# Performance work log

Measured on AMD Instinct MI355X. Metric: run time of the kernel, lower is better.

## Reference

```python
import jax, jax.numpy as jnp
import numpy as np

WINDOW_SIZE = 11
SIGMA = 1.5
CHANNEL = 3


def _gaussian_window(window_size, sigma, channel):
    x = np.arange(window_size, dtype=np.float32)
    g = np.exp(-((x - window_size // 2) ** 2) / (2.0 * sigma ** 2))
    g = g / g.sum()
    w2d = np.outer(g, g).astype(np.float32)  # (ws, ws)
    # depthwise kernel: (C, 1, ws, ws) in OIHW with feature_group_count=C
    return jnp.asarray(np.broadcast_to(w2d, (channel, 1, window_size, window_size)).copy())


def _dwconv(x, w, pad):
    # x: (N, C, H, W), w: (C, 1, kh, kw), depthwise 'same' conv
    return jax.lax.conv_general_dilated(
        x, w, window_strides=(1, 1), padding=[(pad, pad), (pad, pad)],
        dimension_numbers=("NCHW", "OIHW", "NCHW"),
        feature_group_count=x.shape[1])


def setup_inputs() -> dict:
    key = jax.random.key(0)
    k1, k2 = jax.random.split(key)
    img1 = jax.random.uniform(k1, (32, 3, 512, 512), dtype=jnp.float32)
    img2 = jax.random.uniform(k2, (32, 3, 512, 512), dtype=jnp.float32)
    window = _gaussian_window(WINDOW_SIZE, SIGMA, CHANNEL)
    return {"img1": img1, "img2": img2, "window": window}


def reference(img1, img2, window):
    pad = WINDOW_SIZE // 2
    mu1 = _dwconv(img1, window, pad)
    mu2 = _dwconv(img2, window, pad)
    mu1_sq = mu1 * mu1
    mu2_sq = mu2 * mu2
    mu1_mu2 = mu1 * mu2
    sigma1_sq = _dwconv(img1 * img1, window, pad) - mu1_sq
    sigma2_sq = _dwconv(img2 * img2, window, pad) - mu2_sq
    sigma12 = _dwconv(img1 * img2, window, pad) - mu1_mu2

    C1 = 0.01 ** 2
    C2 = 0.03 ** 2
    C3 = C2 / 2.0

    a1 = jnp.abs(sigma1_sq)
    a2 = jnp.abs(sigma2_sq)
    s1 = jnp.sqrt(a1)
    s2 = jnp.sqrt(a2)

    L = (2.0 * mu1_mu2 + C1) / (mu1_sq + mu2_sq + C1)
    C = (2.0 * s1 * s2 + C2) / (a1 + a2 + C2)
    S = (sigma12 + C3) / (s1 * s2 + C3)

    return (L.mean(), C.mean(), S.mean())
```

## Files before the change

### kernel.cpp

```cpp
#include <hip/hip_runtime.h>
#include <math.h>

#define IMG 512
#define PLANES 96
#define XS_W 54
#define NXS 10
#define YS_H 128
#define NYS 4
#define WPB 4
#define NBLK ((PLANES * NXS * NYS) / WPB)
#define INV_NPIX (1.0 / 25165824.0)


static __device__ __forceinline__ float rflf(float x) {
    return __int_as_float(__builtin_amdgcn_readfirstlane(__float_as_int(x)));
}

static __device__ __forceinline__ float dpp_shr1(float x) {
    return __int_as_float(__builtin_amdgcn_mov_dpp(__float_as_int(x), 0x138, 0xF, 0xF, true));
}
static __device__ __forceinline__ float dpp_shl1(float x) {
    return __int_as_float(__builtin_amdgcn_mov_dpp(__float_as_int(x), 0x130, 0xF, 0xF, true));
}

template<int P, int BSEL, bool EMIT>
__device__ __forceinline__ void row_step(
    int T, int y0, bool col_ok,
    const float* __restrict__ p1, const float* __restrict__ p2,
    float& xe1, float& xe2, float& xo1, float& xo2,
    const float (&g)[11],
    float (&A)[5][11], bool out_ok, float& sL, float& sC, float& sS)
{
    const int t = T + P;
    float& x1r = BSEL ? xo1 : xe1;
    float& x2r = BSEL ? xo2 : xe2;
    const int gy2 = y0 - 3 + t;
    float nx1 = 0.f, nx2 = 0.f;
    if (col_ok && (unsigned)gy2 < IMG) {
        int off = gy2 * IMG;
        nx1 = p1[off];
        nx2 = p2[off];
    }
    const float x1 = x1r, x2 = x2r;
    float a4 = dpp_shr1(x1), b4 = dpp_shr1(x2);
    float a3 = dpp_shr1(a4), b3 = dpp_shr1(b4);
    float a2 = dpp_shr1(a3), b2r = dpp_shr1(b3);
    float a1 = dpp_shr1(a2), b1r = dpp_shr1(b2r);
    float a0 = dpp_shr1(a1), b0 = dpp_shr1(b1r);
    float t1 = g[0] * a0, t2 = g[0] * b0;
    float H1 = t1, H2 = t2;
    float H11 = t1 * a0, H22 = t2 * b0, H12 = t1 * b0;
#define HACC(J, AJ, BJ)                                   \
    t1 = g[J] * (AJ); t2 = g[J] * (BJ);                   \
    H1 += t1; H2 += t2;                                   \
    H11 = fmaf(t1, (AJ), H11);                            \
    H22 = fmaf(t2, (BJ), H22);                            \
    H12 = fmaf(t1, (BJ), H12);
    HACC(1, a1, b1r)
    HACC(2, a2, b2r)
    HACC(3, a3, b3)
    HACC(4, a4, b4)
    HACC(5, x1, x2)
    float ar = dpp_shl1(x1), br = dpp_shl1(x2);
    HACC(6, ar, br)
    ar = dpp_shl1(ar); br = dpp_shl1(br);
    HACC(7, ar, br)
    ar = dpp_shl1(ar); br = dpp_shl1(br);
    HACC(8, ar, br)
    ar = dpp_shl1(ar); br = dpp_shl1(br);
    HACC(9, ar, br)
    ar = dpp_shl1(ar); br = dpp_shl1(br);
    HACC(10, ar, br)
#undef HACC
    #pragma unroll
    for (int j = 0; j < 11; ++j) {
        const int s = (P + j + 1) % 11;
        float w = g[10 - j];
        if (j == 10) {
            A[0][s] = w * H1;
            A[1][s] = w * H2;
            A[2][s] = w * H11;
            A[3][s] = w * H22;
            A[4][s] = w * H12;
        } else {
            A[0][s] = fmaf(w, H1,  A[0][s]);
            A[1][s] = fmaf(w, H2,  A[1][s]);
            A[2][s] = fmaf(w, H11, A[2][s]);
            A[3][s] = fmaf(w, H22, A[3][s]);
            A[4][s] = fmaf(w, H12, A[4][s]);
        }
    }
    if (EMIT) {
        const int es = (P + 1) % 11;
        float mu1 = A[0][es], mu2 = A[1][es];
        float x11 = A[2][es], x22 = A[3][es], x12 = A[4][es];
        float mu1s = mu1 * mu1, mu2s = mu2 * mu2, mu12 = mu1 * mu2;
        float v1 = x11 - mu1s, v2 = x22 - mu2s, v12 = x12 - mu12;
        float q1 = fabsf(v1), q2 = fabsf(v2);
        float q12 = sqrtf(q1 * q2);
        const float C1 = 1e-4f, C2 = 9e-4f, C3 = 4.5e-4f;
        float eL = __fdividef(2.f * mu12 + C1, mu1s + mu2s + C1);
        float eC = __fdividef(2.f * q12 + C2, q1 + q2 + C2);
        float eS = __fdividef(v12 + C3, q12 + C3);
        if (out_ok) { sL += eL; sC += eC; sS += eS; }
    }
    x1r = nx1; x2r = nx2;
}

#define RS(Tc, Pc, Bc, Ec) \
    row_step<Pc, Bc, Ec>(Tc, y0, col_ok, p1, p2, xe1, xe2, xo1, xo2, g, A, out_ok, sL, sC, sS)

__global__ __launch_bounds__(256, 4) void ssim_main(
    const float* __restrict__ img1, const float* __restrict__ img2,
    const float* __restrict__ win, float4* __restrict__ part)
{
    const int lane = threadIdx.x & 63;
    const int widx = threadIdx.x >> 6;
    const int wid  = blockIdx.x * WPB + widx;
    const int plane = wid / (NXS * NYS);
    const int rem   = wid % (NXS * NYS);
    const int ys = rem / NXS, xs = rem % NXS;
    const int x0 = xs * XS_W;
    const int y0 = ys * YS_H;
    const int col = x0 - 5 + lane;
    const bool col_ok = (unsigned)col < IMG;
    const bool out_ok = (lane >= 5) && (lane <= 58) && col_ok;

    float g[11];
    #pragma unroll
    for (int j = 0; j < 11; ++j) g[j] = rflf(sqrtf(win[j * 12]));

    const float* p1 = img1 + (size_t)plane * (IMG * IMG) + col;
    const float* p2 = img2 + (size_t)plane * (IMG * IMG) + col;

    float xe1 = 0.f, xe2 = 0.f, xo1 = 0.f, xo2 = 0.f;
    {
        int gy = y0 - 5;
        if (col_ok && (unsigned)gy < IMG) { xe1 = p1[gy * IMG]; xe2 = p2[gy * IMG]; }
        gy = y0 - 4;
        if (col_ok && (unsigned)gy < IMG) { xo1 = p1[gy * IMG]; xo2 = p2[gy * IMG]; }
    }

    float A[5][11];
    #pragma unroll
    for (int q = 0; q < 5; ++q)
        #pragma unroll
        for (int s = 0; s < 11; ++s) A[q][s] = 0.f;

    float sL = 0.f, sC = 0.f, sS = 0.f;

    RS(0, 0, 0, false);
    RS(0, 1, 1, false);
    RS(0, 2, 0, false);
    RS(0, 3, 1, false);
    RS(0, 4, 0, false);
    RS(0, 5, 1, false);
    RS(0, 6, 0, false);
    RS(0, 7, 1, false);
    RS(0, 8, 0, false);
    RS(0, 9, 1, false);
    RS(0, 10, 0, true);

    #pragma unroll 1
    for (int T = 11; T < 121; T += 22) {
        RS(T, 0, 1, true);
        RS(T, 1, 0, true);
        RS(T, 2, 1, true);
        RS(T, 3, 0, true);
        RS(T, 4, 1, true);
        RS(T, 5, 0, true);
        RS(T, 6, 1, true);
        RS(T, 7, 0, true);
        RS(T, 8, 1, true);
        RS(T, 9, 0, true);
        RS(T, 10, 1, true);
        RS(T + 11, 0, 0, true);
        RS(T + 11, 1, 1, true);
        RS(T + 11, 2, 0, true);
        RS(T + 11, 3, 1, true);
        RS(T + 11, 4, 0, true);
        RS(T + 11, 5, 1, true);
        RS(T + 11, 6, 0, true);
        RS(T + 11, 7, 1, true);
        RS(T + 11, 8, 0, true);
        RS(T + 11, 9, 1, true);
        RS(T + 11, 10, 0, true);
    }
    RS(121, 0, 1, true);
    RS(121, 1, 0, true);
    RS(121, 2, 1, true);
    RS(121, 3, 0, true);
    RS(121, 4, 1, true);
    RS(121, 5, 0, true);
    RS(121, 6, 1, true);
    RS(121, 7, 0, true);
    RS(121, 8, 1, true);
    RS(121, 9, 0, true);
    RS(121, 10, 1, true);
    RS(132, 0, 0, true);
    RS(132, 1, 1, true);
    RS(132, 2, 0, true);
    RS(132, 3, 1, true);
    RS(132, 4, 0, true);
    RS(132, 5, 1, true);

    #pragma unroll
    for (int off = 32; off > 0; off >>= 1) {
        sL += __shfl_down(sL, off, 64);
        sC += __shfl_down(sC, off, 64);
        sS += __shfl_down(sS, off, 64);
    }
    __shared__ float red[WPB][4];
    if (lane == 0) { red[widx][0] = sL; red[widx][1] = sC; red[widx][2] = sS; }
    __syncthreads();
    if (threadIdx.x == 0) {
        float L = 0.f, C = 0.f, S = 0.f;
        #pragma unroll
        for (int w = 0; w < WPB; ++w) { L += red[w][0]; C += red[w][1]; S += red[w][2]; }
        part[blockIdx.x] = make_float4(L, C, S, 0.f);
    }
}

__global__ void ssim_fin(const float4* __restrict__ part, float* __restrict__ out) {
    const int t = threadIdx.x;
    double L = 0.0, C = 0.0, S = 0.0;
    for (int i = t; i < NBLK; i += 256) {
        float4 p = part[i];
        L += (double)p.x; C += (double)p.y; S += (double)p.z;
    }
    __shared__ double red[256][3];
    red[t][0] = L; red[t][1] = C; red[t][2] = S;
    __syncthreads();
    for (int s = 128; s > 0; s >>= 1) {
        if (t < s) {
            red[t][0] += red[t + s][0];
            red[t][1] += red[t + s][1];
            red[t][2] += red[t + s][2];
        }
        __syncthreads();
    }
    if (t < 3) out[t] = (float)(red[0][t] * INV_NPIX);
}

extern "C" void kernel_launch(void* const* d_in, const int* in_sizes, int n_in,
                              void* d_out, int out_size, void* d_ws, size_t ws_size,
                              hipStream_t stream) {
    const float* img1 = (const float*)d_in[0];
    const float* img2 = (const float*)d_in[1];
    const float* win  = (const float*)d_in[2];
    float* out = (float*)d_out;
    float4* part = (float4*)d_ws;

    ssim_main<<<NBLK, 64 * WPB, 0, stream>>>(img1, img2, win, part);
    ssim_fin<<<1, 256, 0, stream>>>(part, out);
}
```

Measured before the change: 380.1 us.

## Halve strip height, use branchless clamped loads with SGPR base, relax launch bounds

Each wave now handles 64 output rows instead of 128, doubling the wave count for more parallelism at the cost of more halo rows reread per strip. Row loads become unconditional: the row and column indices are clamped and the loaded value is multiplied by a 0/1 mask, with the plane base and y0 made wave-uniform through readfirstlane. This is meant to drop per-row branches and let loads use scalar base addressing. The launch-bounds occupancy hint drops from 4 to 3, giving the compiler more registers per thread.

```diff
diff --git a/kernel.cpp b/kernel.cpp
--- a/kernel.cpp
+++ b/kernel.cpp
@@ -5,8 +5,8 @@
 #define PLANES 96
 #define XS_W 54
 #define NXS 10
-#define YS_H 128
-#define NYS 4
+#define YS_H 64
+#define NYS 8
 #define WPB 4
 #define NBLK ((PLANES * NXS * NYS) / WPB)
 #define INV_NPIX (1.0 / 25165824.0)
@@ -25,8 +25,9 @@
 
 template<int P, int BSEL, bool EMIT>
 __device__ __forceinline__ void row_step(
-    int T, int y0, bool col_ok,
-    const float* __restrict__ p1, const float* __restrict__ p2,
+    int T, int y0s,
+    const float* __restrict__ b1, const float* __restrict__ b2,
+    unsigned colc, float colokf,
     float& xe1, float& xe2, float& xo1, float& xo2,
     const float (&g)[11],
     float (&A)[5][11], bool out_ok, float& sL, float& sC, float& sS)
@@ -34,13 +35,15 @@
     const int t = T + P;
     float& x1r = BSEL ? xo1 : xe1;
     float& x2r = BSEL ? xo2 : xe2;
-    const int gy2 = y0 - 3 + t;
-    float nx1 = 0.f, nx2 = 0.f;
-    if (col_ok && (unsigned)gy2 < IMG) {
-        int off = gy2 * IMG;
-        nx1 = p1[off];
-        nx2 = p2[off];
-    }
+    const int gy = y0s - 3 + t;
+    const int gyc = gy < 0 ? 0 : (gy > IMG - 1 ? IMG - 1 : gy);
+    const float rowf = ((unsigned)gy < IMG) ? 1.f : 0.f;
+    const unsigned roff = (unsigned)(gyc * IMG);
+    float r1 = b1[roff + colc];
+    float r2 = b2[roff + colc];
+    const float mask = colokf * rowf;
+    float nx1 = r1 * mask;
+    float nx2 = r2 * mask;
     const float x1 = x1r, x2 = x2r;
     float a4 = dpp_shr1(x1), b4 = dpp_shr1(x2);
     float a3 = dpp_shr1(a4), b3 = dpp_shr1(b4);
@@ -108,9 +111,9 @@
 }
 
 #define RS(Tc, Pc, Bc, Ec) \
-    row_step<Pc, Bc, Ec>(Tc, y0, col_ok, p1, p2, xe1, xe2, xo1, xo2, g, A, out_ok, sL, sC, sS)
-
-__global__ __launch_bounds__(256, 4) void ssim_main(
+    row_step<Pc, Bc, Ec>(Tc, y0s, b1, b2, colc, colokf, xe1, xe2, xo1, xo2, g, A, out_ok, sL, sC, sS)
+
+__global__ __launch_bounds__(256, 3) void ssim_main(
     const float* __restrict__ img1, const float* __restrict__ img2,
     const float* __restrict__ win, float4* __restrict__ part)
 {
@@ -125,20 +128,34 @@
     const int col = x0 - 5 + lane;
     const bool col_ok = (unsigned)col < IMG;
     const bool out_ok = (lane >= 5) && (lane <= 58) && col_ok;
+    const unsigned colc = (unsigned)(col < 0 ? 0 : (col > IMG - 1 ? IMG - 1 : col));
+    const float colokf = col_ok ? 1.f : 0.f;
+
+    const int y0s = __builtin_amdgcn_readfirstlane(y0);
+    const int plane_u = __builtin_amdgcn_readfirstlane(plane);
+    const float* b1 = img1 + (size_t)plane_u * (IMG * IMG);
+    const float* b2 = img2 + (size_t)plane_u * (IMG * IMG);
 
     float g[11];
     #pragma unroll
     for (int j = 0; j < 11; ++j) g[j] = rflf(sqrtf(win[j * 12]));
 
-    const float* p1 = img1 + (size_t)plane * (IMG * IMG) + col;
-    const float* p2 = img2 + (size_t)plane * (IMG * IMG) + col;
-
-    float xe1 = 0.f, xe2 = 0.f, xo1 = 0.f, xo2 = 0.f;
+    float xe1, xe2, xo1, xo2;
     {
-        int gy = y0 - 5;
-        if (col_ok && (unsigned)gy < IMG) { xe1 = p1[gy * IMG]; xe2 = p2[gy * IMG]; }
-        gy = y0 - 4;
-        if (col_ok && (unsigned)gy < IMG) { xo1 = p1[gy * IMG]; xo2 = p2[gy * IMG]; }
+        int gy = y0s - 5;
+        int gyc = gy < 0 ? 0 : gy;
+        float rowf = ((unsigned)gy < IMG) ? 1.f : 0.f;
+        float m = colokf * rowf;
+        unsigned roff = (unsigned)(gyc * IMG);
+        xe1 = b1[roff + colc] * m;
+        xe2 = b2[roff + colc] * m;
+        gy = y0s - 4;
+        gyc = gy < 0 ? 0 : gy;
+        rowf = ((unsigned)gy < IMG) ? 1.f : 0.f;
+        m = colokf * rowf;
+        roff = (unsigned)(gyc * IMG);
+        xo1 = b1[roff + colc] * m;
+        xo2 = b2[roff + colc] * m;
     }
 
     float A[5][11];
@@ -162,7 +179,7 @@
     RS(0, 10, 0, true);
 
     #pragma unroll 1
-    for (int T = 11; T < 121; T += 22) {
+    for (int T = 11; T < 55; T += 22) {
         RS(T, 0, 1, true);
         RS(T, 1, 0, true);
         RS(T, 2, 1, true);
@@ -186,23 +203,25 @@
         RS(T + 11, 9, 1, true);
         RS(T + 11, 10, 0, true);
     }
-    RS(121, 0, 1, true);
-    RS(121, 1, 0, true);
-    RS(121, 2, 1, true);
-    RS(121, 3, 0, true);
-    RS(121, 4, 1, true);
-    RS(121, 5, 0, true);
-    RS(121, 6, 1, true);
-    RS(121, 7, 0, true);
-    RS(121, 8, 1, true);
-    RS(121, 9, 0, true);
-    RS(121, 10, 1, true);
-    RS(132, 0, 0, true);
-    RS(132, 1, 1, true);
-    RS(132, 2, 0, true);
-    RS(132, 3, 1, true);
-    RS(132, 4, 0, true);
-    RS(132, 5, 1, true);
+    RS(55, 0, 1, true);
+    RS(55, 1, 0, true);
+    RS(55, 2, 1, true);
+    RS(55, 3, 0, true);
+    RS(55, 4, 1, true);
+    RS(55, 5, 0, true);
+    RS(55, 6, 1, true);
+    RS(55, 7, 0, true);
+    RS(55, 8, 1, true);
+    RS(55, 9, 0, true);
+    RS(55, 10, 1, true);
+    RS(66, 0, 0, true);
+    RS(66, 1, 1, true);
+    RS(66, 2, 0, true);
+    RS(66, 3, 1, true);
+    RS(66, 4, 0, true);
+    RS(66, 5, 1, true);
+    RS(66, 6, 0, true);
+    RS(66, 7, 1, true);
 
     #pragma unroll
     for (int off = 32; off > 0; off >>= 1) {
```

Result: faster. 312.7 us (-17.7%).
